# Kernel optimization log

Measured on AMD Instinct MI355X. Metric: run time of the kernel, lower is better.

## Reference

```python
import jax, jax.numpy as jnp
import numpy as np
import math

D_MODEL = 128
N_HEADS = 8
HEAD_DIM = D_MODEL // N_HEADS


def setup_inputs() -> dict:
    key = jax.random.key(0)
    ks = jax.random.split(key, 16)
    B, N, D = 8, 1024, D_MODEL
    s = 1.0 / math.sqrt(D)
    inp = {
        "x": jax.random.normal(ks[0], (B, N, D), dtype=jnp.float32),
        "adj_mask": jax.random.randint(ks[1], (B, N, N), 0, 2, dtype=jnp.int32),
        "edge_weights": jax.random.uniform(ks[2], (B, N, N), dtype=jnp.float32),
        "Wq": jax.random.normal(ks[3], (D, D), dtype=jnp.float32) * s,
        "bq": jnp.zeros((D,), jnp.float32),
        "Wk": jax.random.normal(ks[4], (D, D), dtype=jnp.float32) * s,
        "bk": jnp.zeros((D,), jnp.float32),
        "Wv": jax.random.normal(ks[5], (D, D), dtype=jnp.float32) * s,
        "bv": jnp.zeros((D,), jnp.float32),
        "Wo": jax.random.normal(ks[6], (D, D), dtype=jnp.float32) * s,
        "bo": jnp.zeros((D,), jnp.float32),
        "We": jax.random.normal(ks[7], (N_HEADS,), dtype=jnp.float32),  # edge_proj weight (n_heads,1) squeezed
        "be": jnp.zeros((N_HEADS,), jnp.float32),                       # edge_proj bias
    }
    return inp


def reference(x, adj_mask, edge_weights, Wq, bq, Wk, bk, Wv, bv, Wo, bo, We, be):
    B, N, D = x.shape
    H, hd = N_HEADS, HEAD_DIM
    scale = math.sqrt(hd)
    # projections -> (B, H, N, hd)
    Q = (x @ Wq + bq).reshape(B, N, H, hd).transpose(0, 2, 1, 3)
    K = (x @ Wk + bk).reshape(B, N, H, hd).transpose(0, 2, 1, 3)
    V = (x @ Wv + bv).reshape(B, N, H, hd).transpose(0, 2, 1, 3)
    # scores (B, H, N, N)
    scores = jnp.einsum('bhnd,bhmd->bhnm', Q, K) / scale
    # edge bias: Linear(1, H) applied per edge, permuted to (B, H, N, N)
    edge_bias = edge_weights[:, None, :, :] * We[None, :, None, None] + be[None, :, None, None]
    scores = scores + edge_bias
    # adjacency masking
    scores = jnp.where(adj_mask[:, None, :, :] == 0, -jnp.inf, scores)
    attn = jax.nn.softmax(scores, axis=-1)  # dropout=0 (eval)
    out = jnp.einsum('bhnm,bhmd->bhnd', attn, V)
    out = out.transpose(0, 2, 1, 3).reshape(B, N, D)
    return out @ Wo + bo
```

## Files before the change

### kernel.cpp

```cpp
#include <hip/hip_runtime.h>
#include <hip/hip_bf16.h>

typedef __attribute__((ext_vector_type(4))) short bf16x4;
typedef __attribute__((ext_vector_type(4))) float f32x4;
typedef __attribute__((ext_vector_type(4))) int i32x4;

#define LOG2E 1.4426950408889634f
#define SMAX 8.0f

static __device__ inline f32x4 mfma16(bf16x4 a, bf16x4 b, f32x4 c) {
  return __builtin_amdgcn_mfma_f32_16x16x16bf16_1k(a, b, c, 0, 0, 0);
}
static __device__ inline ushort f2bfu(float f) {
  __hip_bfloat16 h = __float2bfloat16(f);
  return *(ushort*)&h;
}
static __device__ __forceinline__ void dma16(const void* g, void* l) {
  __builtin_amdgcn_global_load_lds(
      (const __attribute__((address_space(1))) void*)g,
      (__attribute__((address_space(3))) void*)l, 16, 0, 0);
}

__global__ __launch_bounds__(256) void gemm_qkv(
    const float* __restrict__ x,
    const float* __restrict__ Wq, const float* __restrict__ bq,
    const float* __restrict__ Wk, const float* __restrict__ bk,
    const float* __restrict__ Wv, const float* __restrict__ bv,
    ushort* __restrict__ Qs, ushort* __restrict__ Kt, ushort* __restrict__ Vt) {
  const int which = blockIdx.x >> 10;
  const int bid = blockIdx.x & 1023;
  const int tid = threadIdx.x;
  const int l = tid & 63, w = tid >> 6;
  const int lm = l & 15, g = l >> 4;
  const int tile = bid * 4 + w;
  const int mt = tile >> 3, nt = tile & 7;
  const int row = mt * 16 + lm;
  const int col = nt * 16 + lm;

  const float* W = (which == 0) ? Wq : (which == 1) ? Wk : Wv;
  const float* bias = (which == 0) ? bq : (which == 1) ? bk : bv;

  f32x4 acc = {0.f, 0.f, 0.f, 0.f};
#pragma unroll
  for (int ks = 0; ks < 8; ++ks) {
    f32x4 av = *(const f32x4*)(x + (size_t)row * 128 + ks * 16 + g * 4);
    bf16x4 a;
    a[0] = (short)f2bfu(av[0]); a[1] = (short)f2bfu(av[1]);
    a[2] = (short)f2bfu(av[2]); a[3] = (short)f2bfu(av[3]);
    const float* wp = W + (size_t)(ks * 16 + g * 4) * 128 + col;
    bf16x4 b;
    b[0] = (short)f2bfu(wp[0]);   b[1] = (short)f2bfu(wp[128]);
    b[2] = (short)f2bfu(wp[256]); b[3] = (short)f2bfu(wp[384]);
    acc = mfma16(a, b, acc);
  }
  const float bv_ = bias[col];
  const float alpha = (which == 0) ? 0.25f * LOG2E : 1.0f;
  float v0 = (acc[0] + bv_) * alpha, v1 = (acc[1] + bv_) * alpha;
  float v2 = (acc[2] + bv_) * alpha, v3 = (acc[3] + bv_) * alpha;
  const int mb = mt * 16;

  if (which == 0) {
    Qs[(size_t)(mb + g * 4 + 0) * 128 + col] = f2bfu(v0);
    Qs[(size_t)(mb + g * 4 + 1) * 128 + col] = f2bfu(v1);
    Qs[(size_t)(mb + g * 4 + 2) * 128 + col] = f2bfu(v2);
    Qs[(size_t)(mb + g * 4 + 3) * 128 + col] = f2bfu(v3);
  } else if (which == 1) {
    const size_t kb = ((size_t)((mb >> 10) * 8 + nt) * 1024 + ((mb & 1023) + g * 4));
    Kt[(kb + 0) * 16 + lm] = f2bfu(v0);
    Kt[(kb + 1) * 16 + lm] = f2bfu(v1);
    Kt[(kb + 2) * 16 + lm] = f2bfu(v2);
    Kt[(kb + 3) * 16 + lm] = f2bfu(v3);
  } else {
    const size_t addr = ((size_t)((mb >> 10) * 8 + nt) * 16 + ((mb & 1023) >> 6)) * 1024
                        + (size_t)lm * 64 + (mb & 63) + g * 4;
    bf16x4 vv;
    vv[0] = (short)f2bfu(v0); vv[1] = (short)f2bfu(v1);
    vv[2] = (short)f2bfu(v2); vv[3] = (short)f2bfu(v3);
    *(bf16x4*)(Vt + addr) = vv;
  }
}

#define BUFB 49152

__global__ __launch_bounds__(512) void attn_kernel(
    const ushort* __restrict__ Qs, const ushort* __restrict__ Kt,
    const ushort* __restrict__ Vt, const int* __restrict__ adj,
    const float* __restrict__ edge, const float* __restrict__ We,
    const float* __restrict__ Wo, const float* __restrict__ bo,
    float* __restrict__ out) {
  __shared__ __align__(16) char smem[2 * BUFB];

  const int tid = threadIdx.x;
  const int l = tid & 63, h = tid >> 6;
  const int lm = l & 15, g = l >> 4;
  const int b = blockIdx.x >> 5;
  const int m0 = (blockIdx.x & 31) * 32;

  const float Weh = We[h] * LOG2E;
  bf16x4 qf0 = *(const bf16x4*)(Qs + ((size_t)b * 1024 + m0 + lm) * 128 + h * 16 + g * 4);
  bf16x4 qf1 = *(const bf16x4*)(Qs + ((size_t)b * 1024 + m0 + 16 + lm) * 128 + h * 16 + g * 4);

  const ushort* kt0 = Kt + ((size_t)b * 8 + h) * 16384 + l * 8;
  const int dv = l >> 3, mv = l & 7;
  const int voff = dv * 64 + (((mv * 2) ^ (dv & 6)) * 4);
  const ushort* vt0 = Vt + ((size_t)b * 8 + h) * 16384 + voff;

  const int hh = h & 3;
  const int d0 = hh * 2, d1 = d0 + 1;
  const int row0 = 4 * d0 + (l >> 4), row1 = 4 * d1 + (l >> 4);
  const int gr0 = (l & 15) ^ ((row0 & 7) << 1);
  const int gr1 = (l & 15) ^ ((row1 & 7) << 1);
  const int* sbase = ((h < 4) ? adj : (const int*)edge)
                     + (size_t)b * 1048576 + (size_t)m0 * 1024;
  const int* ssrc0 = sbase + (size_t)row0 * 1024 + gr0 * 4;
  const int* ssrc1 = sbase + (size_t)row1 * 1024 + gr1 * 4;

  char* kdst = smem + h * 2048;
  char* vdst = smem + 16384 + h * 2048;
  char* sreg = smem + ((h < 4) ? 32768 : 40960);
  char* sdst0 = sreg + d0 * 1024;
  char* sdst1 = sreg + d1 * 1024;

  float lsum0 = 0.f, lsum1 = 0.f;
  f32x4 oacc0 = {0.f, 0.f, 0.f, 0.f}, oacc1 = {0.f, 0.f, 0.f, 0.f};
  const f32x4 cinit = {-SMAX, -SMAX, -SMAX, -SMAX};

  auto stage = [&](int T) {
    const int bo_ = (T & 1) * BUFB;
    const ushort* ks = kt0 + (size_t)T * 1024;
    const ushort* vs = vt0 + (size_t)T * 1024;
    dma16(ks,        kdst + bo_);
    dma16(ks + 512,  kdst + bo_ + 1024);
    dma16(vs,        vdst + bo_);
    dma16(vs + 512,  vdst + bo_ + 1024);
    dma16(ssrc0 + T * 64, sdst0 + bo_);
    dma16(ssrc1 + T * 64, sdst1 + bo_);
  };

  auto compute = [&](int bi) {
    const char* base = smem + bi * BUFB;
    const char* kls = base + h * 2048;
    const char* vls = base + 16384 + h * 2048;
    const int* als = (const int*)(base + 32768);
    const int* els = (const int*)(base + 40960);
    const int xorv = (lm & 7) << 3;

    bf16x4 kf[4], vfr[4];
#pragma unroll
    for (int t = 0; t < 4; ++t) {
      kf[t]  = *(const bf16x4*)(kls + (t * 16 + lm) * 32 + g * 8);
      vfr[t] = *(const bf16x4*)(vls + lm * 128 + (((t * 4 + g) ^ (lm & 6)) * 8));
    }
#pragma unroll
    for (int s = 0; s < 2; ++s) {
      const bf16x4 qf = s ? qf1 : qf0;
      f32x4 st[4];
#pragma unroll
      for (int t = 0; t < 4; ++t) st[t] = mfma16(kf[t], qf, cinit);
      float lacc = 0.f;
      f32x4 oac = s ? oacc1 : oacc0;
#pragma unroll
      for (int t = 0; t < 4; ++t) {
        const int ci = (t * 16 + g * 4) ^ xorv;
        const int ro = (16 * s + lm) * 64;
        const i32x4 a4 = *(const i32x4*)(als + ro + ci);
        const i32x4 e4i = *(const i32x4*)(els + ro + ci);
        const f32x4 e4 = *(const f32x4*)&e4i;
        bf16x4 pf4;
#pragma unroll
        for (int j = 0; j < 4; ++j) {
          float p = __builtin_amdgcn_exp2f(fmaf(e4[j], Weh, st[t][j]));
          p = (a4[j] == 0) ? 0.f : p;
          lacc += p;
          pf4[j] = (short)f2bfu(p);
        }
        oac = mfma16(vfr[t], pf4, oac);
      }
      if (s) { oacc1 = oac; lsum1 += lacc; } else { oacc0 = oac; lsum0 += lacc; }
    }
  };

  stage(0);
  stage(1);

  for (int ct = 0; ct < 15; ++ct) {
    asm volatile("s_waitcnt vmcnt(6)" ::: "memory");
    __builtin_amdgcn_s_barrier();
    __builtin_amdgcn_sched_barrier(0);
    compute(ct & 1);
    __builtin_amdgcn_s_barrier();
    __builtin_amdgcn_sched_barrier(0);
    if (ct < 14) stage(ct + 2);
  }
  asm volatile("s_waitcnt vmcnt(0)" ::: "memory");
  __builtin_amdgcn_s_barrier();
  __builtin_amdgcn_sched_barrier(0);
  compute(1);

  lsum0 += __shfl_xor(lsum0, 16, 64);
  lsum0 += __shfl_xor(lsum0, 32, 64);
  lsum1 += __shfl_xor(lsum1, 16, 64);
  lsum1 += __shfl_xor(lsum1, 32, 64);
  const float inv0 = 1.0f / lsum0, inv1 = 1.0f / lsum1;

  __syncthreads();
  ushort* aot = (ushort*)smem;
  {
    bf16x4 ov;
    ov[0] = (short)f2bfu(oacc0[0] * inv0);
    ov[1] = (short)f2bfu(oacc0[1] * inv0);
    ov[2] = (short)f2bfu(oacc0[2] * inv0);
    ov[3] = (short)f2bfu(oacc0[3] * inv0);
    *(bf16x4*)(aot + (lm) * 132 + h * 16 + g * 4) = ov;
    ov[0] = (short)f2bfu(oacc1[0] * inv1);
    ov[1] = (short)f2bfu(oacc1[1] * inv1);
    ov[2] = (short)f2bfu(oacc1[2] * inv1);
    ov[3] = (short)f2bfu(oacc1[3] * inv1);
    *(bf16x4*)(aot + (16 + lm) * 132 + h * 16 + g * 4) = ov;
  }
  __syncthreads();

  f32x4 acc0 = {0.f, 0.f, 0.f, 0.f}, acc1 = {0.f, 0.f, 0.f, 0.f};
#pragma unroll
  for (int ks = 0; ks < 8; ++ks) {
    const float* wp = Wo + (size_t)(ks * 16 + g * 4) * 128 + h * 16 + lm;
    bf16x4 bfr;
    bfr[0] = (short)f2bfu(wp[0]);   bfr[1] = (short)f2bfu(wp[128]);
    bfr[2] = (short)f2bfu(wp[256]); bfr[3] = (short)f2bfu(wp[384]);
    bf16x4 a0 = *(const bf16x4*)(aot + lm * 132 + ks * 16 + g * 4);
    bf16x4 a1 = *(const bf16x4*)(aot + (16 + lm) * 132 + ks * 16 + g * 4);
    acc0 = mfma16(a0, bfr, acc0);
    acc1 = mfma16(a1, bfr, acc1);
  }
  const float bv = bo[h * 16 + lm];
  float* op0 = out + ((size_t)b * 1024 + m0 + g * 4) * 128 + h * 16 + lm;
  float* op1 = op0 + 16 * 128;
  op0[0 * 128] = acc0[0] + bv;
  op0[1 * 128] = acc0[1] + bv;
  op0[2 * 128] = acc0[2] + bv;
  op0[3 * 128] = acc0[3] + bv;
  op1[0 * 128] = acc1[0] + bv;
  op1[1 * 128] = acc1[1] + bv;
  op1[2 * 128] = acc1[2] + bv;
  op1[3 * 128] = acc1[3] + bv;
}

extern "C" void kernel_launch(void* const* d_in, const int* in_sizes, int n_in,
                              void* d_out, int out_size, void* d_ws, size_t ws_size,
                              hipStream_t stream) {
  const float* x   = (const float*)d_in[0];
  const int*   adj = (const int*)d_in[1];
  const float* ew  = (const float*)d_in[2];
  const float* Wq  = (const float*)d_in[3];
  const float* bq  = (const float*)d_in[4];
  const float* Wk  = (const float*)d_in[5];
  const float* bk  = (const float*)d_in[6];
  const float* Wv  = (const float*)d_in[7];
  const float* bv  = (const float*)d_in[8];
  const float* Wo  = (const float*)d_in[9];
  const float* bo  = (const float*)d_in[10];
  const float* We  = (const float*)d_in[11];

  const size_t MN = (size_t)8 * 1024 * 128;
  ushort* Qs = (ushort*)d_ws;
  ushort* Kt = Qs + MN;
  ushort* Vt = Kt + MN;

  gemm_qkv<<<3072, 256, 0, stream>>>(x, Wq, bq, Wk, bk, Wv, bv, Qs, Kt, Vt);
  attn_kernel<<<256, 512, 0, stream>>>(Qs, Kt, Vt, adj, ew, We, Wo, bo, (float*)d_out);
}
```

Before: 52.44 us.

## Pre-transpose QKV weights to bf16 and compute softmax row sums via MFMA

Adds a small kernel that converts Wq/Wk/Wv to bf16 in transposed layout, so the QKV GEMM loads B fragments as one vector instead of four strided fp32 loads with conversions. In the attention kernel the per-lane scalar accumulation of probabilities, and the cross-lane shuffle reduction, are replaced by an extra MFMA against a ones vector that yields row sums directly. This trades VALU adds and shuffles for extra matrix-core work, plus one extra kernel launch and workspace. The row sums now come from bf16-rounded probabilities, which matches what is multiplied into V.

Result: slower. 63.54 us (+21.2%).

```diff
diff --git a/kernel.cpp b/kernel.cpp
--- a/kernel.cpp
+++ b/kernel.cpp
@@ -21,11 +21,20 @@
       (__attribute__((address_space(3))) void*)l, 16, 0, 0);
 }
 
+__global__ __launch_bounds__(128) void prep_w(
+    const float* __restrict__ Wq, const float* __restrict__ Wk,
+    const float* __restrict__ Wv, ushort* __restrict__ Wt) {
+  const int m = blockIdx.x >> 7;
+  const int c = blockIdx.x & 127;
+  const int k = threadIdx.x;
+  const float* W = (m == 0) ? Wq : (m == 1) ? Wk : Wv;
+  Wt[((size_t)m * 128 + c) * 128 + k] = f2bfu(W[(size_t)k * 128 + c]);
+}
+
 __global__ __launch_bounds__(256) void gemm_qkv(
-    const float* __restrict__ x,
-    const float* __restrict__ Wq, const float* __restrict__ bq,
-    const float* __restrict__ Wk, const float* __restrict__ bk,
-    const float* __restrict__ Wv, const float* __restrict__ bv,
+    const float* __restrict__ x, const ushort* __restrict__ Wt,
+    const float* __restrict__ bq, const float* __restrict__ bk,
+    const float* __restrict__ bv,
     ushort* __restrict__ Qs, ushort* __restrict__ Kt, ushort* __restrict__ Vt) {
   const int which = blockIdx.x >> 10;
   const int bid = blockIdx.x & 1023;
@@ -37,8 +46,8 @@
   const int row = mt * 16 + lm;
   const int col = nt * 16 + lm;
 
-  const float* W = (which == 0) ? Wq : (which == 1) ? Wk : Wv;
   const float* bias = (which == 0) ? bq : (which == 1) ? bk : bv;
+  const ushort* wt = Wt + ((size_t)which * 128 + col) * 128;
 
   f32x4 acc = {0.f, 0.f, 0.f, 0.f};
 #pragma unroll
@@ -47,10 +56,7 @@
     bf16x4 a;
     a[0] = (short)f2bfu(av[0]); a[1] = (short)f2bfu(av[1]);
     a[2] = (short)f2bfu(av[2]); a[3] = (short)f2bfu(av[3]);
-    const float* wp = W + (size_t)(ks * 16 + g * 4) * 128 + col;
-    bf16x4 b;
-    b[0] = (short)f2bfu(wp[0]);   b[1] = (short)f2bfu(wp[128]);
-    b[2] = (short)f2bfu(wp[256]); b[3] = (short)f2bfu(wp[384]);
+    bf16x4 b = *(const bf16x4*)(wt + ks * 16 + g * 4);
     acc = mfma16(a, b, acc);
   }
   const float bv_ = bias[col];
@@ -121,9 +127,11 @@
   char* sdst0 = sreg + d0 * 1024;
   char* sdst1 = sreg + d1 * 1024;
 
-  float lsum0 = 0.f, lsum1 = 0.f;
   f32x4 oacc0 = {0.f, 0.f, 0.f, 0.f}, oacc1 = {0.f, 0.f, 0.f, 0.f};
+  f32x4 lacc0 = {0.f, 0.f, 0.f, 0.f}, lacc1 = {0.f, 0.f, 0.f, 0.f};
   const f32x4 cinit = {-SMAX, -SMAX, -SMAX, -SMAX};
+  const short ONE = (short)0x3F80;
+  const bf16x4 ones = {ONE, ONE, ONE, ONE};
 
   auto stage = [&](int T) {
     const int bo_ = (T & 1) * BUFB;
@@ -157,8 +165,8 @@
       f32x4 st[4];
 #pragma unroll
       for (int t = 0; t < 4; ++t) st[t] = mfma16(kf[t], qf, cinit);
-      float lacc = 0.f;
       f32x4 oac = s ? oacc1 : oacc0;
+      f32x4 pac = s ? lacc1 : lacc0;
 #pragma unroll
       for (int t = 0; t < 4; ++t) {
         const int ci = (t * 16 + g * 4) ^ xorv;
@@ -171,12 +179,12 @@
         for (int j = 0; j < 4; ++j) {
           float p = __builtin_amdgcn_exp2f(fmaf(e4[j], Weh, st[t][j]));
           p = (a4[j] == 0) ? 0.f : p;
-          lacc += p;
           pf4[j] = (short)f2bfu(p);
         }
         oac = mfma16(vfr[t], pf4, oac);
+        pac = mfma16(ones,   pf4, pac);
       }
-      if (s) { oacc1 = oac; lsum1 += lacc; } else { oacc0 = oac; lsum0 += lacc; }
+      if (s) { oacc1 = oac; lacc1 = pac; } else { oacc0 = oac; lacc0 = pac; }
     }
   };
 
@@ -197,11 +205,8 @@
   __builtin_amdgcn_sched_barrier(0);
   compute(1);
 
-  lsum0 += __shfl_xor(lsum0, 16, 64);
-  lsum0 += __shfl_xor(lsum0, 32, 64);
-  lsum1 += __shfl_xor(lsum1, 16, 64);
-  lsum1 += __shfl_xor(lsum1, 32, 64);
-  const float inv0 = 1.0f / lsum0, inv1 = 1.0f / lsum1;
+  const float inv0 = 1.0f / lacc0[0];
+  const float inv1 = 1.0f / lacc1[0];
 
   __syncthreads();
   ushort* aot = (ushort*)smem;
@@ -265,7 +270,9 @@
   ushort* Qs = (ushort*)d_ws;
   ushort* Kt = Qs + MN;
   ushort* Vt = Kt + MN;
-
-  gemm_qkv<<<3072, 256, 0, stream>>>(x, Wq, bq, Wk, bk, Wv, bv, Qs, Kt, Vt);
+  ushort* Wt = Vt + MN;
+
+  prep_w<<<384, 128, 0, stream>>>(Wq, Wk, Wv, Wt);
+  gemm_qkv<<<3072, 256, 0, stream>>>(x, Wt, bq, bk, bv, Qs, Kt, Vt);
   attn_kernel<<<256, 512, 0, stream>>>(Qs, Kt, Vt, adj, ew, We, Wo, bo, (float*)d_out);
 }
```
